# Kernel optimization log

Hardware: AMD Instinct MI355X
Metric: run time of the kernel (lower is better)

## Reference

```python
import jax, jax.numpy as jnp
import numpy as np

FEATURE_DIM = 256
HEADS = 8


def setup_inputs() -> dict:
    key = jax.random.key(0)
    ks = jax.random.split(key, 9)
    d, h = FEATURE_DIM, HEADS
    b, n = 4, 4096
    s_in = 1.0 / np.sqrt(d)
    s_out = 1.0 / np.sqrt(d * h)
    return {
        "x": jax.random.normal(ks[0], (b, n, d), dtype=jnp.float32),
        "Wq": jax.random.uniform(ks[1], (d, d * h), jnp.float32, -s_in, s_in),
        "bq": jax.random.uniform(ks[2], (d * h,), jnp.float32, -s_in, s_in),
        "Wk": jax.random.uniform(ks[3], (d, d * h), jnp.float32, -s_in, s_in),
        "bk": jax.random.uniform(ks[4], (d * h,), jnp.float32, -s_in, s_in),
        "Wv": jax.random.uniform(ks[5], (d, d * h), jnp.float32, -s_in, s_in),
        "bv": jax.random.uniform(ks[6], (d * h,), jnp.float32, -s_in, s_in),
        "Wo": jax.random.uniform(ks[7], (d * h, d), jnp.float32, -s_out, s_out),
        "bo": jax.random.uniform(ks[8], (d,), jnp.float32, -s_out, s_out),
    }


def reference(x, Wq, bq, Wk, bk, Wv, bv, Wo, bo):
    b, n, d = x.shape
    h = HEADS
    scale = d ** (-0.5)
    # projections: (b, n, h, d) -- note: NO head transpose, matching original
    q = (x @ Wq + bq).reshape(b, n, h, d)
    k = (x @ Wk + bk).reshape(b, n, h, d)
    v = (x @ Wv + bv).reshape(b, n, h, d)
    # attention is head-vs-head per token: (b, n, h, h)
    attn = jnp.einsum("bnhd,bngd->bnhg", q, k) * scale
    attn = jax.nn.softmax(attn, axis=-1)
    out = jnp.einsum("bnhg,bngd->bnhd", attn, v).reshape(b, n, h * d)
    return out @ Wo + bo
```

## Files before the change

kernel.cpp:

```cpp
#include <hip/hip_runtime.h>
#include <hip/hip_bf16.h>
#include <math.h>

typedef __bf16 bf16;
typedef __bf16 bf16x4 __attribute__((ext_vector_type(4)));
typedef __bf16 bf16x8 __attribute__((ext_vector_type(8)));
typedef float f32x4 __attribute__((ext_vector_type(4)));
typedef unsigned int u32;
typedef u32 __attribute__((address_space(1))) gu32;
typedef u32 __attribute__((address_space(3))) lu32;

#define TOK   16384
#define D_    256
#define HD    2048
#define VN    2048

#define GLDS16(g, l) __builtin_amdgcn_global_load_lds((gu32*)(g), (lu32*)(l), 16, 0, 0)
#define WAIT_VM(n)  __builtin_amdgcn_s_waitcnt(0x0F70 | (n))
#define WAIT_LGKM0  __builtin_amdgcn_s_waitcnt(0xC07F)
#define BAR() do { __builtin_amdgcn_s_barrier(); __builtin_amdgcn_sched_barrier(0); } while (0)
#define SCHEDFENCE() __builtin_amdgcn_sched_barrier(0)

__device__ __forceinline__ void transpose_body(
    const void* __restrict__ src, bf16* __restrict__ dst, int R, int C,
    int tc, int tr, int f, int mode, float (*tile)[33])
{
    int lx = threadIdx.x & 31, ly = threadIdx.x >> 5;
    for (int i = 0; i < 4; i++) {
        int r = ly + i * 8;
        size_t idx = (size_t)(tr + r) * C + tc + lx;
        tile[r][lx] = f ? ((const float*)src)[idx] : (float)((const bf16*)src)[idx];
    }
    __syncthreads();
    for (int i = 0; i < 4; i++) {
        int r = ly + i * 8;
        int k = tr + lx;
        int n = tc + r;
        size_t di;
        if (mode == 1)
            di = (size_t)n * 2048 + ((k & 255) << 3) + (k >> 8);
        else if (mode == 2)
            di = (size_t)(4096 + ((n & 255) << 3) + (n >> 8)) * 256 + k;
        else if (mode == 3)
            di = (size_t)((((n & 255) >> 3) << 7) + ((n >> 8) << 3) + (n & 7)) * 256 + k;
        else if (mode == 4)
            di = (size_t)((((n & 255) >> 3) << 7) + 64 + ((n >> 8) << 3) + (n & 7)) * 256 + k;
        else
            di = (size_t)n * R + k;
        dst[di] = (bf16)tile[lx][r];
    }
}

__global__ __launch_bounds__(256) void prep(
    const void* __restrict__ x,
    const void* __restrict__ Wq, const void* __restrict__ bq,
    const void* __restrict__ Wk, const void* __restrict__ bk,
    const void* __restrict__ Wv, const void* __restrict__ bv,
    const void* __restrict__ Wo, const void* __restrict__ bo,
    bf16* __restrict__ xb, bf16* __restrict__ WTI, bf16* __restrict__ WoT,
    bf16* __restrict__ bqkv, bf16* __restrict__ bob)
{
    __shared__ float tile[32][33];
    __shared__ int sflag;
    int tid = threadIdx.x;
    if (tid == 0) sflag = 0;
    __syncthreads();
    {
        float v = fabsf((float)((const bf16*)x)[2 * tid]);
        if (!(v < 1e4f)) sflag = 1;
    }
    __syncthreads();
    int f = sflag;
    int b = blockIdx.x;

    if (b < 4096) {
        int i = b * 256 + tid;
        bf16x4 o;
        if (f) { f32x4 v = ((const f32x4*)x)[i]; for (int e = 0; e < 4; e++) o[e] = (bf16)v[e]; }
        else   { o = ((const bf16x4*)x)[i]; }
        ((bf16x4*)xb)[i] = o;
    } else if (b < 4121) {
        int i = (b - 4096) * 256 + tid;
        if (i < 6400) {
            const void* src; bf16* dst = bqkv; int off, woff;
            if (i < 2048) {
                src = bq; off = i;
                int d = off & 255, h = off >> 8;
                woff = ((d >> 3) << 7) + (h << 3) + (d & 7);
            } else if (i < 4096) {
                src = bk; off = i - 2048;
                int d = off & 255, h = off >> 8;
                woff = ((d >> 3) << 7) + 64 + (h << 3) + (d & 7);
            } else if (i < 6144) {
                src = bv; off = i - 4096;
                woff = 4096 + ((off & 255) << 3) + (off >> 8);
            } else {
                src = bo; dst = bob; off = i - 6144; woff = off;
            }
            float v = f ? ((const float*)src)[off] : (float)((const bf16*)src)[off];
            dst[woff] = (bf16)v;
        }
        __syncthreads();
    } else if (b < 5657) {
        int idx = b - 4121;
        int tx = idx & 63, rest = idx >> 6;
        int ty = rest & 7, tz = rest >> 3;
        const void* src = (tz == 0) ? Wq : (tz == 1) ? Wk : Wv;
        int mode = (tz == 0) ? 3 : (tz == 1) ? 4 : 2;
        transpose_body(src, WTI, 256, 2048, tx * 32, ty * 32, f, mode, tile);
    } else {
        int idx = b - 5657;
        int tx = idx & 7, ty = idx >> 3;
        transpose_body(Wo, WoT, 2048, 256, tx * 32, ty * 32, f, 1, tile);
    }
}

__global__ __launch_bounds__(256) void v_proj(
    const bf16* __restrict__ X, const bf16* __restrict__ WT,
    const bf16* __restrict__ bI, bf16* __restrict__ vout)
{
    __shared__ char smem[36864];
    bf16* As = (bf16*)smem;
    bf16* Bs = (bf16*)(smem + 16384);
    int m0 = blockIdx.y * 128, n0 = blockIdx.x * 128;
    int tid = threadIdx.x, wave = tid >> 6, lane = tid & 63;
    int wm = (wave >> 1) * 64, wn = (wave & 1) * 64;
    int mrow = lane & 15, quad = lane >> 4;
    int lrow8 = lane >> 3, lslot = lane & 7;

    f32x4 acc[4][4] = {};
    for (int k0 = 0; k0 < D_; k0 += 64) {
        __syncthreads();
        for (int i = 0; i < 4; i++) {
            int rbase = wave * 32 + i * 8;
            int row = rbase + lrow8;
            int gc = lslot ^ (row & 7);
            GLDS16(&X[(size_t)(m0 + row) * D_ + k0 + gc * 8], &As[rbase * 64]);
            GLDS16(&WT[(size_t)(n0 + row) * D_ + k0 + gc * 8], &Bs[rbase * 64]);
        }
        __syncthreads();
        for (int kk = 0; kk < 64; kk += 32) {
            int slot = (((kk >> 3) + quad) ^ (mrow & 7)) * 8;
            bf16x8 af[4], bfv[4];
            for (int mt = 0; mt < 4; mt++)
                af[mt] = *(const bf16x8*)&As[(wm + mt * 16 + mrow) * 64 + slot];
            for (int nt = 0; nt < 4; nt++)
                bfv[nt] = *(const bf16x8*)&Bs[(wn + nt * 16 + mrow) * 64 + slot];
            for (int mt = 0; mt < 4; mt++)
                for (int nt = 0; nt < 4; nt++)
                    acc[mt][nt] = __builtin_amdgcn_mfma_f32_16x16x32_bf16(
                        bfv[nt], af[mt], acc[mt][nt], 0, 0, 0);
        }
    }

    __syncthreads();
    bf16* ep = (bf16*)smem + wave * (64 * 72);
    for (int mt = 0; mt < 4; mt++) {
        for (int nt = 0; nt < 4; nt++) {
            int col = n0 + wn + nt * 16 + quad * 4;
            bf16x4 bb = *(const bf16x4*)&bI[col];
            bf16x4 o;
            for (int r = 0; r < 4; r++) o[r] = (bf16)(acc[mt][nt][r] + (float)bb[r]);
            *(bf16x4*)&ep[(mt * 16 + mrow) * 72 + nt * 16 + quad * 4] = o;
        }
    }
    __syncthreads();
    for (int i = 0; i < 8; i++) {
        int r = i * 8 + (lane >> 3);
        int cb = (lane & 7) * 8;
        bf16x8 val = *(const bf16x8*)&ep[r * 72 + cb];
        *(bf16x8*)&vout[(size_t)(m0 + wm + r) * VN + n0 + wn + cb] = val;
    }
}

__global__ __launch_bounds__(512, 2) void qk_score(
    const bf16* __restrict__ X, const bf16* __restrict__ WTI,
    const bf16* __restrict__ bI, float* __restrict__ P)
{
    __shared__ bf16 Ws[8][2][16 * 256];
    __shared__ bf16 qkh[64 * 136];
    int tid = threadIdx.x, wave = tid >> 6, lane = tid & 63;
    int mrow = lane & 15, quad = lane >> 4;
    int h = lane >> 3, g = lane & 7;
    int t0 = blockIdx.x * 64;
    bf16* wsbase = &Ws[0][0][0];

#pragma unroll
    for (int i = 0; i < 4; i++) {
        int row = (i * 8 + wave) * 2 + (lane >> 5);
        int sl = lane & 31;
        int gc = (sl & 24) | ((sl & 7) ^ (row & 7));
        GLDS16(&X[(size_t)(t0 + row) * 256 + gc * 8], &wsbase[(i * 8 + wave) * 512]);
    }
    WAIT_VM(0);
    BAR();
    bf16x8 areg[4][8];
#pragma unroll
    for (int mt = 0; mt < 4; mt++)
#pragma unroll
        for (int ks = 0; ks < 8; ks++) {
            int arow = mt * 16 + mrow;
            int sl = ks * 4 + quad;
            int ph = (sl & 24) | ((sl & 7) ^ (arow & 7));
            areg[mt][ks] = *(const bf16x8*)&wsbase[arow * 256 + ph * 8];
        }
    WAIT_LGKM0;
    BAR();

    bf16* wsw = &Ws[wave][0][0];
    const bf16* wsrc = WTI + (size_t)(wave * 16) * 256;
#define QK_STAGE(IT, BUF) {                                                    \
        const bf16* s_ = wsrc + (size_t)(IT) * 32768;                          \
        bf16* d_ = wsw + (BUF) * 4096;                                         \
        _Pragma("unroll")                                                      \
        for (int j = 0; j < 8; j++) {                                          \
            int row = j * 2 + (lane >> 5);                                     \
            int sl = lane & 31;                                                \
            int gc = (sl & 24) | ((sl & 7) ^ (row & 7));                       \
            GLDS16(&s_[(size_t)row * 256 + gc * 8], &d_[j * 512]);             \
        } }
    QK_STAGE(0, 0)
    QK_STAGE(1, 1)

    float S[8] = {};

    for (int it = 0; it < 32; it++) {
        if (it == 31) { WAIT_VM(0); } else { WAIT_VM(8); }
        const bf16* wb = wsw + (it & 1) * 4096;
        bf16x8 bvv[8];
#pragma unroll
        for (int ks = 0; ks < 8; ks++) {
            int sl = ks * 4 + quad;
            int ph = (sl & 24) | ((sl & 7) ^ (mrow & 7));
            bvv[ks] = *(const bf16x8*)&wb[mrow * 256 + ph * 8];
        }
        WAIT_LGKM0;
        SCHEDFENCE();
        if (it < 30) QK_STAGE(it + 2, it & 1)

        f32x4 acc[4] = {};
#pragma unroll
        for (int ks = 0; ks < 8; ks++)
#pragma unroll
            for (int mt = 0; mt < 4; mt++)
                acc[mt] = __builtin_amdgcn_mfma_f32_16x16x32_bf16(
                    bvv[ks], areg[mt][ks], acc[mt], 0, 0, 0);

        bf16x4 bb = *(const bf16x4*)&bI[it * 128 + wave * 16 + quad * 4];
#pragma unroll
        for (int mt = 0; mt < 4; mt++) {
            int t = mt * 16 + mrow;
            bf16x4 o;
#pragma unroll
            for (int r = 0; r < 4; r++) o[r] = (bf16)(acc[mt][r] + (float)bb[r]);
            *(bf16x4*)&qkh[t * 136 + wave * 16 + quad * 4] = o;
        }
        WAIT_LGKM0;
        BAR();

#pragma unroll
        for (int u = 0; u < 8; u++) {
            int t = wave * 8 + u;
            bf16x8 qv = *(const bf16x8*)&qkh[t * 136 + h * 8];
            bf16x8 kv = *(const bf16x8*)&qkh[t * 136 + 64 + g * 8];
            float a = 0.f;
#pragma unroll
            for (int e = 0; e < 8; e++) a += (float)qv[e] * (float)kv[e];
            S[u] += a;
        }
        WAIT_LGKM0;
        BAR();
    }
#undef QK_STAGE

#pragma unroll
    for (int u = 0; u < 8; u++) {
        int t = t0 + wave * 8 + u;
        float sc = S[u] * 0.0625f;
        float m = sc;
        for (int off = 1; off < 8; off <<= 1) m = fmaxf(m, __shfl_xor(m, off, 8));
        float p = __expf(sc - m);
        float sum = p;
        for (int off = 1; off < 8; off <<= 1) sum += __shfl_xor(sum, off, 8);
        P[(size_t)t * 64 + lane] = p / sum;
    }
}

__global__ __launch_bounds__(256) void out_fused(
    const bf16* __restrict__ vb, const bf16* __restrict__ WoT,
    const float* __restrict__ P, const bf16* __restrict__ bob,
    float* __restrict__ outp)
{
    __shared__ bf16 Bs[2][256 * 64];
    __shared__ bf16 Vs[2][32 * 64];
    int m0 = blockIdx.x * 32;
    int tid = threadIdx.x, wave = tid >> 6, lane = tid & 63;
    int wm = (wave >> 1) * 16, wn = (wave & 1) * 128;
    int mrow = lane & 15, quad = lane >> 4;
    int t = wm + mrow, ts = t & 7;
    int sl8 = lane >> 3, sl = lane & 7;

    float Pv[64];
    {
        const float* pr = P + (size_t)(m0 + t) * 64;
#pragma unroll
        for (int j = 0; j < 16; j++) {
            f32x4 v4 = *(const f32x4*)&pr[j * 4];
            Pv[4 * j + 0] = v4[0]; Pv[4 * j + 1] = v4[1];
            Pv[4 * j + 2] = v4[2]; Pv[4 * j + 3] = v4[3];
        }
    }

    f32x4 acc[8] = {};
    {
        int tt = (wave << 3) + sl8;
        GLDS16(&vb[(size_t)(m0 + tt) * VN + ((sl ^ (tt & 7)) << 3)],
               &Vs[0][wave * 512]);
#pragma unroll
        for (int i = 0; i < 8; i++) {
            int n = (wave << 6) + (i << 3) + sl8;
            GLDS16(&WoT[(size_t)n * HD + ((sl ^ (n & 7)) << 3)],
                   &Bs[0][((wave << 6) + (i << 3)) << 6]);
        }
    }

    for (int c = 0; c < 32; c++) {
        __syncthreads();
        if (c < 31) {
            int cc = c + 1, bb = cc & 1;
            int tt = (wave << 3) + sl8;
            GLDS16(&vb[(size_t)(m0 + tt) * VN + cc * 64 + ((sl ^ (tt & 7)) << 3)],
                   &Vs[bb][wave * 512]);
#pragma unroll
            for (int i = 0; i < 8; i++) {
                int n = (wave << 6) + (i << 3) + sl8;
                GLDS16(&WoT[(size_t)n * HD + cc * 64 + ((sl ^ (n & 7)) << 3)],
                       &Bs[bb][((wave << 6) + (i << 3)) << 6]);
            }
        }
        const bf16* Vb = Vs[c & 1];
        const bf16* Bb = Bs[c & 1];

        bf16x8 vf0 = *(const bf16x8*)&Vb[(t << 6) + ((quad ^ ts) << 3)];
        bf16x8 vf1 = *(const bf16x8*)&Vb[(t << 6) + (((quad + 4) ^ ts) << 3)];
        float v0f[8], v1f[8];
#pragma unroll
        for (int e = 0; e < 8; e++) { v0f[e] = (float)vf0[e]; v1f[e] = (float)vf1[e]; }
        bf16x8 af0, af1;
#pragma unroll
        for (int hh = 0; hh < 8; hh++) {
            float a0 = 0.f, a1 = 0.f;
#pragma unroll
            for (int gg = 0; gg < 8; gg++) {
                a0 += Pv[hh * 8 + gg] * v0f[gg];
                a1 += Pv[hh * 8 + gg] * v1f[gg];
            }
            af0[hh] = (bf16)a0; af1[hh] = (bf16)a1;
        }
#pragma unroll
        for (int nt = 0; nt < 8; nt++) {
            bf16x8 bv = *(const bf16x8*)&Bb[(wn + nt * 16 + mrow) * 64
                            + ((quad ^ (mrow & 7)) << 3)];
            acc[nt] = __builtin_amdgcn_mfma_f32_16x16x32_bf16(bv, af0, acc[nt], 0, 0, 0);
        }
#pragma unroll
        for (int nt = 0; nt < 8; nt++) {
            bf16x8 bv = *(const bf16x8*)&Bb[(wn + nt * 16 + mrow) * 64
                            + (((4 + quad) ^ (mrow & 7)) << 3)];
            acc[nt] = __builtin_amdgcn_mfma_f32_16x16x32_bf16(bv, af1, acc[nt], 0, 0, 0);
        }
    }

    int row = m0 + wm + mrow;
#pragma unroll
    for (int nt = 0; nt < 8; nt++) {
        int col = wn + nt * 16 + quad * 4;
        bf16x4 bb = *(const bf16x4*)&bob[col];
        f32x4 o;
        for (int r = 0; r < 4; r++) o[r] = acc[nt][r] + (float)bb[r];
        *(f32x4*)&outp[(size_t)row * D_ + col] = o;
    }
}

extern "C" void kernel_launch(void* const* d_in, const int* in_sizes, int n_in,
                              void* d_out, int out_size, void* d_ws, size_t ws_size,
                              hipStream_t stream)
{
    const void* x  = d_in[0];
    const void* Wq = d_in[1];
    const void* bq = d_in[2];
    const void* Wk = d_in[3];
    const void* bk = d_in[4];
    const void* Wv = d_in[5];
    const void* bv = d_in[6];
    const void* Wo = d_in[7];
    const void* bo = d_in[8];
    float* out = (float*)d_out;

    char* ws = (char*)d_ws;
    bf16*  vbuf = (bf16*)ws;
    bf16*  WTI  = (bf16*)(ws + 67108864);
    bf16*  WoT  = (bf16*)(ws + 70254592);
    bf16*  xb   = (bf16*)(ws + 71303168);
    bf16*  bqkv = (bf16*)(ws + 79691776);
    bf16*  bob  = (bf16*)(ws + 79704064);
    float* Pbuf = (float*)(ws + 79704576);

    prep<<<6169, 256, 0, stream>>>(x, Wq, bq, Wk, bk, Wv, bv, Wo, bo,
                                   xb, WTI, WoT, bqkv, bob);
    qk_score<<<256, 512, 0, stream>>>(xb, WTI, bqkv, Pbuf);
    v_proj<<<dim3(16, 128), 256, 0, stream>>>(xb, WTI + 4096 * 256, bqkv + 4096, vbuf);
    out_fused<<<512, 256, 0, stream>>>(vbuf, WoT, Pbuf, bob, out);
}
```

Before: 241.4 us.

## Split QK score reduction across two blocks and move softmax into output kernel

The qk_score kernel now splits the 256-wide feature reduction into two halves handled by separate blocks, doubling the grid from 256 to 512 blocks so more of the GPU is busy. Each block writes partial raw scores to a buffer, and out_fused sums the two partials, scales them and applies the per-head softmax in registers. Weight staging drops from double buffering to a single buffer to cut LDS use, and the qk staging tile gets an XOR swizzle instead of padding to avoid bank conflicts. In exchange the pipeline stalls on each weight load, the X tile is loaded and projected twice, and the score traffic to global memory doubles.

```diff
diff --git a/kernel.cpp b/kernel.cpp
--- a/kernel.cpp
+++ b/kernel.cpp
@@ -173,17 +173,19 @@
     }
 }
 
-__global__ __launch_bounds__(512, 2) void qk_score(
+__global__ __launch_bounds__(512, 4) void qk_score(
     const bf16* __restrict__ X, const bf16* __restrict__ WTI,
-    const bf16* __restrict__ bI, float* __restrict__ P)
-{
-    __shared__ bf16 Ws[8][2][16 * 256];
-    __shared__ bf16 qkh[64 * 136];
+    const bf16* __restrict__ bI, float* __restrict__ Sbuf)
+{
+    __shared__ bf16 Ws[8][16 * 256];
+    __shared__ bf16 qkh[64 * 128];
     int tid = threadIdx.x, wave = tid >> 6, lane = tid & 63;
     int mrow = lane & 15, quad = lane >> 4;
     int h = lane >> 3, g = lane & 7;
-    int t0 = blockIdx.x * 64;
-    bf16* wsbase = &Ws[0][0][0];
+    int bid = blockIdx.x;
+    int t0 = (bid >> 1) * 64;
+    int dh = bid & 1;
+    bf16* wsbase = &Ws[0][0];
 
 #pragma unroll
     for (int i = 0; i < 4; i++) {
@@ -207,36 +209,34 @@
     WAIT_LGKM0;
     BAR();
 
-    bf16* wsw = &Ws[wave][0][0];
+    bf16* wsw = &Ws[wave][0];
     const bf16* wsrc = WTI + (size_t)(wave * 16) * 256;
-#define QK_STAGE(IT, BUF) {                                                    \
-        const bf16* s_ = wsrc + (size_t)(IT) * 32768;                          \
-        bf16* d_ = wsw + (BUF) * 4096;                                         \
+#define QK_STAGE(GIT) {                                                        \
+        const bf16* s_ = wsrc + (size_t)(GIT) * 32768;                         \
         _Pragma("unroll")                                                      \
         for (int j = 0; j < 8; j++) {                                          \
             int row = j * 2 + (lane >> 5);                                     \
             int sl = lane & 31;                                                \
             int gc = (sl & 24) | ((sl & 7) ^ (row & 7));                       \
-            GLDS16(&s_[(size_t)row * 256 + gc * 8], &d_[j * 512]);             \
+            GLDS16(&s_[(size_t)row * 256 + gc * 8], &wsw[j * 512]);            \
         } }
-    QK_STAGE(0, 0)
-    QK_STAGE(1, 1)
+    QK_STAGE(dh * 16)
 
     float S[8] = {};
 
-    for (int it = 0; it < 32; it++) {
-        if (it == 31) { WAIT_VM(0); } else { WAIT_VM(8); }
-        const bf16* wb = wsw + (it & 1) * 4096;
+    for (int it = 0; it < 16; it++) {
+        int git = dh * 16 + it;
+        WAIT_VM(0);
         bf16x8 bvv[8];
 #pragma unroll
         for (int ks = 0; ks < 8; ks++) {
             int sl = ks * 4 + quad;
             int ph = (sl & 24) | ((sl & 7) ^ (mrow & 7));
-            bvv[ks] = *(const bf16x8*)&wb[mrow * 256 + ph * 8];
+            bvv[ks] = *(const bf16x8*)&wsw[mrow * 256 + ph * 8];
         }
         WAIT_LGKM0;
         SCHEDFENCE();
-        if (it < 30) QK_STAGE(it + 2, it & 1)
+        if (it < 15) QK_STAGE(git + 1)
 
         f32x4 acc[4] = {};
 #pragma unroll
@@ -246,14 +246,15 @@
                 acc[mt] = __builtin_amdgcn_mfma_f32_16x16x32_bf16(
                     bvv[ks], areg[mt][ks], acc[mt], 0, 0, 0);
 
-        bf16x4 bb = *(const bf16x4*)&bI[it * 128 + wave * 16 + quad * 4];
+        bf16x4 bb = *(const bf16x4*)&bI[git * 128 + wave * 16 + quad * 4];
 #pragma unroll
         for (int mt = 0; mt < 4; mt++) {
             int t = mt * 16 + mrow;
             bf16x4 o;
 #pragma unroll
             for (int r = 0; r < 4; r++) o[r] = (bf16)(acc[mt][r] + (float)bb[r]);
-            *(bf16x4*)&qkh[t * 136 + wave * 16 + quad * 4] = o;
+            int g8 = (wave * 4 + quad) ^ ((t & 7) << 1);
+            *(bf16x4*)((char*)qkh + t * 256 + g8 * 8) = o;
         }
         WAIT_LGKM0;
         BAR();
@@ -261,8 +262,10 @@
 #pragma unroll
         for (int u = 0; u < 8; u++) {
             int t = wave * 8 + u;
-            bf16x8 qv = *(const bf16x8*)&qkh[t * 136 + h * 8];
-            bf16x8 kv = *(const bf16x8*)&qkh[t * 136 + 64 + g * 8];
+            int s = (t & 7) << 1;
+            const char* base = (const char*)qkh + t * 256;
+            bf16x8 qv = *(const bf16x8*)(base + ((h * 2) ^ s) * 8);
+            bf16x8 kv = *(const bf16x8*)(base + ((16 + g * 2) ^ s) * 8);
             float a = 0.f;
 #pragma unroll
             for (int e = 0; e < 8; e++) a += (float)qv[e] * (float)kv[e];
@@ -276,19 +279,13 @@
 #pragma unroll
     for (int u = 0; u < 8; u++) {
         int t = t0 + wave * 8 + u;
-        float sc = S[u] * 0.0625f;
-        float m = sc;
-        for (int off = 1; off < 8; off <<= 1) m = fmaxf(m, __shfl_xor(m, off, 8));
-        float p = __expf(sc - m);
-        float sum = p;
-        for (int off = 1; off < 8; off <<= 1) sum += __shfl_xor(sum, off, 8);
-        P[(size_t)t * 64 + lane] = p / sum;
+        Sbuf[(size_t)dh * TOK * 64 + (size_t)t * 64 + lane] = S[u];
     }
 }
 
 __global__ __launch_bounds__(256) void out_fused(
     const bf16* __restrict__ vb, const bf16* __restrict__ WoT,
-    const float* __restrict__ P, const bf16* __restrict__ bob,
+    const float* __restrict__ Sbuf, const bf16* __restrict__ bob,
     float* __restrict__ outp)
 {
     __shared__ bf16 Bs[2][256 * 64];
@@ -302,12 +299,26 @@
 
     float Pv[64];
     {
-        const float* pr = P + (size_t)(m0 + t) * 64;
+        const float* p0 = Sbuf + (size_t)(m0 + t) * 64;
+        const float* p1 = p0 + (size_t)TOK * 64;
 #pragma unroll
         for (int j = 0; j < 16; j++) {
-            f32x4 v4 = *(const f32x4*)&pr[j * 4];
-            Pv[4 * j + 0] = v4[0]; Pv[4 * j + 1] = v4[1];
-            Pv[4 * j + 2] = v4[2]; Pv[4 * j + 3] = v4[3];
+            f32x4 a = *(const f32x4*)&p0[j * 4];
+            f32x4 b = *(const f32x4*)&p1[j * 4];
+            for (int e = 0; e < 4; e++) Pv[4 * j + e] = (a[e] + b[e]) * 0.0625f;
+        }
+#pragma unroll
+        for (int hh = 0; hh < 8; hh++) {
+            float m = Pv[hh * 8];
+            for (int e = 1; e < 8; e++) m = fmaxf(m, Pv[hh * 8 + e]);
+            float sum = 0.f;
+            for (int e = 0; e < 8; e++) {
+                float p = __expf(Pv[hh * 8 + e] - m);
+                Pv[hh * 8 + e] = p;
+                sum += p;
+            }
+            float inv = 1.f / sum;
+            for (int e = 0; e < 8; e++) Pv[hh * 8 + e] *= inv;
         }
     }
 
@@ -404,11 +415,11 @@
     bf16*  xb   = (bf16*)(ws + 71303168);
     bf16*  bqkv = (bf16*)(ws + 79691776);
     bf16*  bob  = (bf16*)(ws + 79704064);
-    float* Pbuf = (float*)(ws + 79704576);
+    float* Sbuf = (float*)(ws + 79704576);
 
     prep<<<6169, 256, 0, stream>>>(x, Wq, bq, Wk, bk, Wv, bv, Wo, bo,
                                    xb, WTI, WoT, bqkv, bob);
-    qk_score<<<256, 512, 0, stream>>>(xb, WTI, bqkv, Pbuf);
+    qk_score<<<512, 512, 0, stream>>>(xb, WTI, bqkv, Sbuf);
     v_proj<<<dim3(16, 128), 256, 0, stream>>>(xb, WTI + 4096 * 256, bqkv + 4096, vbuf);
-    out_fused<<<512, 256, 0, stream>>>(vbuf, WoT, Pbuf, bob, out);
-}
+    out_fused<<<512, 256, 0, stream>>>(vbuf, WoT, Sbuf, bob, out);
+}
```

Result: slower. 424.2 us (+75.7%).

## Halve qk_score token tile, single-buffer weights, swizzle qkh LDS layout

Applied to the files above, without the earlier changes.

The qk_score kernel now handles 32 tokens per block instead of 64, so it launches 512 blocks and requests 4 blocks per CU. The weight staging buffer drops from double to single buffering to cut LDS use. The q/k scratch tile gets an XOR-swizzled layout to avoid LDS bank conflicts. This trades load/compute overlap and twice the weight reloads per token for more blocks, more occupancy and better spread across CUs.

```diff
diff --git a/kernel.cpp b/kernel.cpp
--- a/kernel.cpp
+++ b/kernel.cpp
@@ -173,30 +173,31 @@
     }
 }
 
-__global__ __launch_bounds__(512, 2) void qk_score(
+__global__ __launch_bounds__(512, 4) void qk_score(
     const bf16* __restrict__ X, const bf16* __restrict__ WTI,
     const bf16* __restrict__ bI, float* __restrict__ P)
 {
-    __shared__ bf16 Ws[8][2][16 * 256];
-    __shared__ bf16 qkh[64 * 136];
+    __shared__ bf16 Ws[8][16 * 256];
+    __shared__ __align__(16) char qkh[32 * 288];
     int tid = threadIdx.x, wave = tid >> 6, lane = tid & 63;
     int mrow = lane & 15, quad = lane >> 4;
     int h = lane >> 3, g = lane & 7;
-    int t0 = blockIdx.x * 64;
-    bf16* wsbase = &Ws[0][0][0];
-
-#pragma unroll
-    for (int i = 0; i < 4; i++) {
-        int row = (i * 8 + wave) * 2 + (lane >> 5);
+    int t0 = blockIdx.x * 32;
+    bf16* wsbase = &Ws[0][0];
+
+#pragma unroll
+    for (int i = 0; i < 2; i++) {
+        int row = i * 16 + wave * 2 + (lane >> 5);
         int sl = lane & 31;
         int gc = (sl & 24) | ((sl & 7) ^ (row & 7));
-        GLDS16(&X[(size_t)(t0 + row) * 256 + gc * 8], &wsbase[(i * 8 + wave) * 512]);
+        GLDS16(&X[(size_t)(t0 + row) * 256 + gc * 8],
+               &wsbase[(i * 16 + wave * 2) * 256]);
     }
     WAIT_VM(0);
     BAR();
-    bf16x8 areg[4][8];
-#pragma unroll
-    for (int mt = 0; mt < 4; mt++)
+    bf16x8 areg[2][8];
+#pragma unroll
+    for (int mt = 0; mt < 2; mt++)
 #pragma unroll
         for (int ks = 0; ks < 8; ks++) {
             int arow = mt * 16 + mrow;
@@ -207,62 +208,62 @@
     WAIT_LGKM0;
     BAR();
 
-    bf16* wsw = &Ws[wave][0][0];
+    bf16* wsw = &Ws[wave][0];
     const bf16* wsrc = WTI + (size_t)(wave * 16) * 256;
-#define QK_STAGE(IT, BUF) {                                                    \
-        const bf16* s_ = wsrc + (size_t)(IT) * 32768;                          \
-        bf16* d_ = wsw + (BUF) * 4096;                                         \
+#define QK_STAGE(GIT) {                                                        \
+        const bf16* s_ = wsrc + (size_t)(GIT) * 32768;                         \
         _Pragma("unroll")                                                      \
         for (int j = 0; j < 8; j++) {                                          \
             int row = j * 2 + (lane >> 5);                                     \
             int sl = lane & 31;                                                \
             int gc = (sl & 24) | ((sl & 7) ^ (row & 7));                       \
-            GLDS16(&s_[(size_t)row * 256 + gc * 8], &d_[j * 512]);             \
+            GLDS16(&s_[(size_t)row * 256 + gc * 8], &wsw[j * 512]);            \
         } }
-    QK_STAGE(0, 0)
-    QK_STAGE(1, 1)
-
-    float S[8] = {};
+    QK_STAGE(0)
+
+    float S[4] = {};
 
     for (int it = 0; it < 32; it++) {
-        if (it == 31) { WAIT_VM(0); } else { WAIT_VM(8); }
-        const bf16* wb = wsw + (it & 1) * 4096;
+        WAIT_VM(0);
         bf16x8 bvv[8];
 #pragma unroll
         for (int ks = 0; ks < 8; ks++) {
             int sl = ks * 4 + quad;
             int ph = (sl & 24) | ((sl & 7) ^ (mrow & 7));
-            bvv[ks] = *(const bf16x8*)&wb[mrow * 256 + ph * 8];
+            bvv[ks] = *(const bf16x8*)&wsw[mrow * 256 + ph * 8];
         }
         WAIT_LGKM0;
         SCHEDFENCE();
-        if (it < 30) QK_STAGE(it + 2, it & 1)
-
-        f32x4 acc[4] = {};
+        if (it < 31) QK_STAGE(it + 1)
+
+        f32x4 acc[2] = {};
 #pragma unroll
         for (int ks = 0; ks < 8; ks++)
 #pragma unroll
-            for (int mt = 0; mt < 4; mt++)
+            for (int mt = 0; mt < 2; mt++)
                 acc[mt] = __builtin_amdgcn_mfma_f32_16x16x32_bf16(
                     bvv[ks], areg[mt][ks], acc[mt], 0, 0, 0);
 
         bf16x4 bb = *(const bf16x4*)&bI[it * 128 + wave * 16 + quad * 4];
 #pragma unroll
-        for (int mt = 0; mt < 4; mt++) {
+        for (int mt = 0; mt < 2; mt++) {
             int t = mt * 16 + mrow;
             bf16x4 o;
 #pragma unroll
             for (int r = 0; r < 4; r++) o[r] = (bf16)(acc[mt][r] + (float)bb[r]);
-            *(bf16x4*)&qkh[t * 136 + wave * 16 + quad * 4] = o;
+            int g8 = (wave * 4 + quad) ^ ((t & 7) << 1);
+            *(bf16x4*)(qkh + t * 288 + g8 * 8) = o;
         }
         WAIT_LGKM0;
         BAR();
 
 #pragma unroll
-        for (int u = 0; u < 8; u++) {
-            int t = wave * 8 + u;
-            bf16x8 qv = *(const bf16x8*)&qkh[t * 136 + h * 8];
-            bf16x8 kv = *(const bf16x8*)&qkh[t * 136 + 64 + g * 8];
+        for (int u = 0; u < 4; u++) {
+            int t = wave * 4 + u;
+            int s = (t & 7) << 1;
+            const char* base = qkh + t * 288;
+            bf16x8 qv = *(const bf16x8*)(base + ((h * 2) ^ s) * 8);
+            bf16x8 kv = *(const bf16x8*)(base + (((16 + g * 2)) ^ s) * 8);
             float a = 0.f;
 #pragma unroll
             for (int e = 0; e < 8; e++) a += (float)qv[e] * (float)kv[e];
@@ -274,8 +275,8 @@
 #undef QK_STAGE
 
 #pragma unroll
-    for (int u = 0; u < 8; u++) {
-        int t = t0 + wave * 8 + u;
+    for (int u = 0; u < 4; u++) {
+        int t = t0 + wave * 4 + u;
         float sc = S[u] * 0.0625f;
         float m = sc;
         for (int off = 1; off < 8; off <<= 1) m = fmaxf(m, __shfl_xor(m, off, 8));
@@ -408,7 +409,7 @@
 
     prep<<<6169, 256, 0, stream>>>(x, Wq, bq, Wk, bk, Wv, bv, Wo, bo,
                                    xb, WTI, WoT, bqkv, bob);
-    qk_score<<<256, 512, 0, stream>>>(xb, WTI, bqkv, Pbuf);
+    qk_score<<<512, 512, 0, stream>>>(xb, WTI, bqkv, Pbuf);
     v_proj<<<dim3(16, 128), 256, 0, stream>>>(xb, WTI + 4096 * 256, bqkv + 4096, vbuf);
     out_fused<<<512, 256, 0, stream>>>(vbuf, WoT, Pbuf, bob, out);
 }
```

Result: slower. 281.5 us (+16.6%).
